# Performance work log

Hardware: AMD Instinct MI355X
Metric: run time of the kernel (lower is better)

Reference implementation:

```python
import jax, jax.numpy as jnp
import numpy as np


def _fwht_last(x):
    """Unnormalized Walsh-Hadamard transform along the last axis (len = power of 2)."""
    n = x.shape[-1]
    h = 1
    while h < n:
        x = x.reshape(*x.shape[:-1], n // (2 * h), 2, h)
        a, b = x[..., 0, :], x[..., 1, :]
        x = jnp.stack([a + b, a - b], axis=-2).reshape(*x.shape[:-3], n)
        h *= 2
    return x


def fwht(x, axis=-1):
    if axis in (-1, x.ndim - 1):
        return _fwht_last(x)
    return jnp.swapaxes(_fwht_last(jnp.swapaxes(x, axis, -1)), axis, -1)


def soft_threshold(x, T):
    return jnp.copysign(jax.nn.relu(jnp.abs(x) - jax.nn.relu(T)), x)


def setup_inputs() -> dict:
    key = jax.random.key(0)
    k1, k2, k3, k4 = jax.random.split(key, 4)
    B, C, H, W_dim = 32, 64, 128, 128
    x = jax.random.normal(k1, (B, C, H, W_dim), dtype=jnp.float32)
    W = jax.random.normal(k2, (C, C), dtype=jnp.float32) * 0.1  # 1x1 conv weight [out,in]
    v = jax.random.uniform(k3, (H, W_dim), dtype=jnp.float32)
    T = jax.random.uniform(k4, (H, W_dim), dtype=jnp.float32) * 0.1
    return {"x": x, "W": W, "v": v, "T": T}


def reference(x, W, v, T):
    H, Wd = x.shape[-2], x.shape[-1]
    # forward 2-D WHT (no padding: H, W already powers of 2)
    f2 = fwht(fwht(x, axis=-1), axis=-2)
    # spectral gate + 1x1 conv (channel mixing)
    f4 = jnp.einsum('oc,bchw->bohw', W, v * f2)
    # soft thresholding
    f6 = soft_threshold(f4, T)
    # inverse 2-D WHT = forward WHT / n along each axis
    y = fwht(fwht(f6, axis=-1), axis=-2) / (H * Wd)
    return y + x  # residual
```

## Files before the change

### kernel.cpp

```cpp
#include <hip/hip_runtime.h>
#include <math.h>

#define HW 16384
#define NPLANE 2048

typedef __bf16 bf16x8 __attribute__((ext_vector_type(8)));
typedef float  f32x4  __attribute__((ext_vector_type(4)));


__device__ __forceinline__ void bf_quad(float4& a) {
    float s0 = a.x + a.y, d0 = a.x - a.y;
    float s1 = a.z + a.w, d1 = a.z - a.w;
    a.x = s0 + s1; a.y = d0 + d1; a.z = s0 - s1; a.w = d0 - d1;
}

__device__ __forceinline__ void bf_pair(float4& a, float4& b) {
    float4 s, d;
    s.x = a.x + b.x; s.y = a.y + b.y; s.z = a.z + b.z; s.w = a.w + b.w;
    d.x = a.x - b.x; d.y = a.y - b.y; d.z = a.z - b.z; d.w = a.w - b.w;
    a = s; b = d;
}

__device__ __forceinline__ void bf_regs3(float4 (&r)[8]) {
    #pragma unroll
    for (int m = 1; m <= 4; m <<= 1) {
        #pragma unroll
        for (int j = 0; j < 8; ++j) {
            if (!(j & m)) bf_pair(r[j], r[j | m]);
        }
    }
}

__device__ __forceinline__ void wht14(const float* __restrict__ src,
                                      float* __restrict__ lds,
                                      float4 (&r)[8], int t) {
    const float4* s4 = reinterpret_cast<const float4*>(src);
    #pragma unroll
    for (int j = 0; j < 8; ++j) r[j] = s4[t + j * 512];
    #pragma unroll
    for (int j = 0; j < 8; ++j) bf_quad(r[j]);
    bf_regs3(r);

    {
        const int physT = (t & 3)
                        + ((((t >> 5) ^ (t >> 4)) & 1) << 4)
                        + (((t >> 6) & 7) << 5)
                        + (((t >> 2) & 7) << 8);
        const int swc = (t >> 2) & 3;
        #pragma unroll
        for (int j = 0; j < 8; ++j) {
            float* b = lds + physT + j * 2048;
            b[(0 ^ swc) << 2] = r[j].x;
            b[(1 ^ swc) << 2] = r[j].y;
            b[(2 ^ swc) << 2] = r[j].z;
            b[(3 ^ swc) << 2] = r[j].w;
        }
    }
    __syncthreads();

    {
        const int baseT = ((t & 63) << 2) + ((t >> 6) << 11);
        int addr[8];
        #pragma unroll
        for (int j = 0; j < 8; ++j) {
            addr[j] = (baseT ^ ((j & 3) << 2) ^ ((j >> 2) << 4)) + (j << 8);
            r[j] = *reinterpret_cast<const float4*>(lds + addr[j]);
        }
        #pragma unroll
        for (int j = 0; j < 8; ++j) bf_quad(r[j]);
        bf_regs3(r);
        #pragma unroll
        for (int j = 0; j < 8; ++j)
            *reinterpret_cast<float4*>(lds + addr[j]) = r[j];
    }
    __syncthreads();

    {
        const int t0 = t & 1, t1 = (t >> 1) & 1, t2 = (t >> 2) & 1;
        const int t3 = (t >> 3) & 1, t4 = (t >> 4) & 1, t5 = (t >> 5) & 1;
        const int cT = t1 + (t2 << 1) + ((t0 ^ t4) << 3)
                     + (t3 << 8) + (t4 << 9) + (t5 << 10) + ((t >> 6) << 11);
        #pragma unroll
        for (int j = 0; j < 8; ++j) {
            const int a = cT + ((((j >> 2) ^ t3)) << 2)
                        + ((j & 1) << 6) + (((j >> 1) & 1) << 7);
            float4 q;
            q.x = lds[a + ((0 ^ t5) << 4)];
            q.y = lds[a + ((1 ^ t5) << 4)];
            q.z = lds[a + ((0 ^ t5) << 4) + (1 << 5)];
            q.w = lds[a + ((1 ^ t5) << 4) + (1 << 5)];
            r[j] = q;
        }
        #pragma unroll
        for (int j = 0; j < 8; ++j) bf_quad(r[j]);
        #pragma unroll
        for (int m = 1; m <= 2; m <<= 1) {
            #pragma unroll
            for (int j = 0; j < 8; ++j) {
                if (!(j & m)) bf_pair(r[j], r[j | m]);
            }
        }
    }
}

__global__ __launch_bounds__(512) void k_wht2d_fwd(const float* __restrict__ x,
                                                   float* __restrict__ out) {
    __shared__ float lds[HW];
    const int t = threadIdx.x;
    const size_t plane = (size_t)blockIdx.x * HW;

    float4 r[8];
    wht14(x + plane, lds, r, t);

    float* dst = out + plane;
    const int dT = ((t & 63) << 1) + ((t >> 6) << 11);
    #pragma unroll
    for (int j = 0; j < 4; ++j) {
        const int jb = dT + ((j & 1) << 9) + ((j >> 1) << 10);
        const float* lo = reinterpret_cast<const float*>(&r[j]);
        const float* hi = reinterpret_cast<const float*>(&r[j + 4]);
        #pragma unroll
        for (int c = 0; c < 4; ++c) {
            const int d = jb + ((c & 1) << 7) + ((c >> 1) << 8);
            float2 o; o.x = lo[c]; o.y = hi[c];
            *reinterpret_cast<float2*>(dst + d) = o;
        }
    }
}

__global__ __launch_bounds__(512) void k_wht2d_inv(float* __restrict__ buf,
                                                   const float* __restrict__ x) {
    __shared__ float lds[HW];
    const int t = threadIdx.x;
    const size_t plane = (size_t)blockIdx.x * HW;

    float4 r[8];
    wht14(buf + plane, lds, r, t);

    float* dst = buf + plane;
    const float* xr = x + plane;
    const float s = 1.0f / 16384.0f;
    const int dT = ((t & 63) << 1) + ((t >> 6) << 11);
    #pragma unroll
    for (int j = 0; j < 4; ++j) {
        const int jb = dT + ((j & 1) << 9) + ((j >> 1) << 10);
        const float* lo = reinterpret_cast<const float*>(&r[j]);
        const float* hi = reinterpret_cast<const float*>(&r[j + 4]);
        #pragma unroll
        for (int c = 0; c < 4; ++c) {
            const int d = jb + ((c & 1) << 7) + ((c >> 1) << 8);
            float2 xv = *reinterpret_cast<const float2*>(xr + d);
            float2 o;
            o.x = lo[c] * s + xv.x;
            o.y = hi[c] * s + xv.y;
            *reinterpret_cast<float2*>(dst + d) = o;
        }
    }
}

__global__ __launch_bounds__(256) void k_mix_mfma(float* __restrict__ buf,
                                                  const float* __restrict__ W,
                                                  const float* __restrict__ v,
                                                  const float* __restrict__ T) {
    __shared__ float Xs[64 * 128];
    const int t = threadIdx.x;
    const int l = t & 63, w = t >> 6;
    const int b  = blockIdx.x >> 7;
    const int p0 = (blockIdx.x & 127) << 7;
    float* base = buf + (size_t)b * 64 * HW + p0;

    bf16x8 A[4][2];
    {
        const int row = l & 15;
        const int kc  = (l >> 4) * 8;
        #pragma unroll
        for (int mt = 0; mt < 4; ++mt) {
            const float* wr = W + (mt * 16 + row) * 64 + kc;
            #pragma unroll
            for (int ks = 0; ks < 2; ++ks) {
                float4 w0 = *reinterpret_cast<const float4*>(wr + ks * 32);
                float4 w1 = *reinterpret_cast<const float4*>(wr + ks * 32 + 4);
                bf16x8 a;
                a[0] = (__bf16)w0.x; a[1] = (__bf16)w0.y;
                a[2] = (__bf16)w0.z; a[3] = (__bf16)w0.w;
                a[4] = (__bf16)w1.x; a[5] = (__bf16)w1.y;
                a[6] = (__bf16)w1.z; a[7] = (__bf16)w1.w;
                A[mt][ks] = a;
            }
        }
    }

    #pragma unroll
    for (int i = 0; i < 8; ++i) {
        const int d  = i * 1024 + t * 4;
        const int c  = d >> 7;
        const int pq = d & 127;
        float4 xv = *reinterpret_cast<const float4*>(base + (size_t)c * HW + pq);
        float4 vv = *reinterpret_cast<const float4*>(v + p0 + pq);
        float4 r;
        r.x = xv.x * vv.x; r.y = xv.y * vv.y;
        r.z = xv.z * vv.z; r.w = xv.w * vv.w;
        const int gc = (c >> 3) & 3;
        *reinterpret_cast<float4*>(Xs + c * 128 + (pq ^ (gc << 4))) = r;
    }
    __syncthreads();

    f32x4 acc[4][2] = {};
    const int n0 = w * 32;
    const int g  = l >> 4;
    #pragma unroll
    for (int nt = 0; nt < 2; ++nt) {
        const int pl = n0 + nt * 16 + (l & 15);
        #pragma unroll
        for (int ks = 0; ks < 2; ++ks) {
            const float* col = Xs + (ks * 32 + g * 8) * 128 + (pl ^ (g << 4));
            bf16x8 bb;
            #pragma unroll
            for (int j = 0; j < 8; ++j) bb[j] = (__bf16)col[j * 128];
            #pragma unroll
            for (int mt = 0; mt < 4; ++mt)
                acc[mt][nt] = __builtin_amdgcn_mfma_f32_16x16x32_bf16(
                    A[mt][ks], bb, acc[mt][nt], 0, 0, 0);
        }
    }

    #pragma unroll
    for (int nt = 0; nt < 2; ++nt) {
        const int p  = p0 + n0 + nt * 16 + (l & 15);
        const float Tp = fmaxf(T[p], 0.0f);
        #pragma unroll
        for (int mt = 0; mt < 4; ++mt) {
            #pragma unroll
            for (int r = 0; r < 4; ++r) {
                const int o = mt * 16 + g * 4 + r;
                float val = acc[mt][nt][r];
                float mag = fmaxf(fabsf(val) - Tp, 0.0f);
                buf[(size_t)b * 64 * HW + (size_t)o * HW + p] = copysignf(mag, val);
            }
        }
    }
}

extern "C" void kernel_launch(void* const* d_in, const int* in_sizes, int n_in,
                              void* d_out, int out_size, void* d_ws, size_t ws_size,
                              hipStream_t stream) {
    const float* x = (const float*)d_in[0];
    const float* W = (const float*)d_in[1];
    const float* v = (const float*)d_in[2];
    const float* T = (const float*)d_in[3];
    float* out = (float*)d_out;

    k_wht2d_fwd<<<NPLANE, 512, 0, stream>>>(x, out);
    k_mix_mfma<<<32 * 128, 256, 0, stream>>>(out, W, v, T);
    k_wht2d_inv<<<NPLANE, 512, 0, stream>>>(out, x);
}
```

Baseline: 151.1 us.

## Process four planes per block with software-prefetch of next plane in WHT kernels

The forward and inverse WHT kernels now handle four 128x128 planes per workgroup, launching 512 blocks instead of 2048. Each iteration loads the next plane into registers while the LDS butterfly phases of the current plane run, and the inverse kernel issues its residual loads early. Barriers become explicit s_barrier calls with lgkmcnt waits and scheduling fences. The aim is to hide global-load latency. In exchange, register pressure goes up (a second 8xfloat4 buffer plus 16 float2 residuals), and with fewer blocks there may be less parallelism to fill the GPU.

```diff
diff --git a/kernel.cpp b/kernel.cpp
--- a/kernel.cpp
+++ b/kernel.cpp
@@ -7,6 +7,13 @@
 typedef __bf16 bf16x8 __attribute__((ext_vector_type(8)));
 typedef float  f32x4  __attribute__((ext_vector_type(4)));
 
+
+__device__ __forceinline__ void wg_barrier() {
+    __builtin_amdgcn_sched_barrier(0);
+    asm volatile("s_waitcnt lgkmcnt(0)");
+    __builtin_amdgcn_s_barrier();
+    __builtin_amdgcn_sched_barrier(0);
+}
 
 __device__ __forceinline__ void bf_quad(float4& a) {
     float s0 = a.x + a.y, d0 = a.x - a.y;
@@ -31,74 +38,67 @@
     }
 }
 
-__device__ __forceinline__ void wht14(const float* __restrict__ src,
-                                      float* __restrict__ lds,
-                                      float4 (&r)[8], int t) {
-    const float4* s4 = reinterpret_cast<const float4*>(src);
-    #pragma unroll
-    for (int j = 0; j < 8; ++j) r[j] = s4[t + j * 512];
+__device__ __forceinline__ void phaseA(float* __restrict__ lds,
+                                       float4 (&r)[8], int t) {
     #pragma unroll
     for (int j = 0; j < 8; ++j) bf_quad(r[j]);
     bf_regs3(r);
-
-    {
-        const int physT = (t & 3)
-                        + ((((t >> 5) ^ (t >> 4)) & 1) << 4)
-                        + (((t >> 6) & 7) << 5)
-                        + (((t >> 2) & 7) << 8);
-        const int swc = (t >> 2) & 3;
+    const int physT = (t & 3)
+                    + ((((t >> 5) ^ (t >> 4)) & 1) << 4)
+                    + (((t >> 6) & 7) << 5)
+                    + (((t >> 2) & 7) << 8);
+    const int swc = (t >> 2) & 3;
+    #pragma unroll
+    for (int j = 0; j < 8; ++j) {
+        float* b = lds + physT + j * 2048;
+        b[(0 ^ swc) << 2] = r[j].x;
+        b[(1 ^ swc) << 2] = r[j].y;
+        b[(2 ^ swc) << 2] = r[j].z;
+        b[(3 ^ swc) << 2] = r[j].w;
+    }
+}
+
+__device__ __forceinline__ void phaseB(float* __restrict__ lds,
+                                       float4 (&r)[8], int t) {
+    const int baseT = ((t & 63) << 2) + ((t >> 6) << 11);
+    int addr[8];
+    #pragma unroll
+    for (int j = 0; j < 8; ++j) {
+        addr[j] = (baseT ^ ((j & 3) << 2) ^ ((j >> 2) << 4)) + (j << 8);
+        r[j] = *reinterpret_cast<const float4*>(lds + addr[j]);
+    }
+    #pragma unroll
+    for (int j = 0; j < 8; ++j) bf_quad(r[j]);
+    bf_regs3(r);
+    #pragma unroll
+    for (int j = 0; j < 8; ++j)
+        *reinterpret_cast<float4*>(lds + addr[j]) = r[j];
+}
+
+__device__ __forceinline__ void phaseC(const float* __restrict__ lds,
+                                       float4 (&r)[8], int t) {
+    const int t0 = t & 1, t1 = (t >> 1) & 1, t2 = (t >> 2) & 1;
+    const int t3 = (t >> 3) & 1, t4 = (t >> 4) & 1, t5 = (t >> 5) & 1;
+    const int cT = t1 + (t2 << 1) + ((t0 ^ t4) << 3)
+                 + (t3 << 8) + (t4 << 9) + (t5 << 10) + ((t >> 6) << 11);
+    #pragma unroll
+    for (int j = 0; j < 8; ++j) {
+        const int a = cT + ((((j >> 2) ^ t3)) << 2)
+                    + ((j & 1) << 6) + (((j >> 1) & 1) << 7);
+        float4 q;
+        q.x = lds[a + ((0 ^ t5) << 4)];
+        q.y = lds[a + ((1 ^ t5) << 4)];
+        q.z = lds[a + ((0 ^ t5) << 4) + (1 << 5)];
+        q.w = lds[a + ((1 ^ t5) << 4) + (1 << 5)];
+        r[j] = q;
+    }
+    #pragma unroll
+    for (int j = 0; j < 8; ++j) bf_quad(r[j]);
+    #pragma unroll
+    for (int m = 1; m <= 2; m <<= 1) {
         #pragma unroll
         for (int j = 0; j < 8; ++j) {
-            float* b = lds + physT + j * 2048;
-            b[(0 ^ swc) << 2] = r[j].x;
-            b[(1 ^ swc) << 2] = r[j].y;
-            b[(2 ^ swc) << 2] = r[j].z;
-            b[(3 ^ swc) << 2] = r[j].w;
-        }
-    }
-    __syncthreads();
-
-    {
-        const int baseT = ((t & 63) << 2) + ((t >> 6) << 11);
-        int addr[8];
-        #pragma unroll
-        for (int j = 0; j < 8; ++j) {
-            addr[j] = (baseT ^ ((j & 3) << 2) ^ ((j >> 2) << 4)) + (j << 8);
-            r[j] = *reinterpret_cast<const float4*>(lds + addr[j]);
-        }
-        #pragma unroll
-        for (int j = 0; j < 8; ++j) bf_quad(r[j]);
-        bf_regs3(r);
-        #pragma unroll
-        for (int j = 0; j < 8; ++j)
-            *reinterpret_cast<float4*>(lds + addr[j]) = r[j];
-    }
-    __syncthreads();
-
-    {
-        const int t0 = t & 1, t1 = (t >> 1) & 1, t2 = (t >> 2) & 1;
-        const int t3 = (t >> 3) & 1, t4 = (t >> 4) & 1, t5 = (t >> 5) & 1;
-        const int cT = t1 + (t2 << 1) + ((t0 ^ t4) << 3)
-                     + (t3 << 8) + (t4 << 9) + (t5 << 10) + ((t >> 6) << 11);
-        #pragma unroll
-        for (int j = 0; j < 8; ++j) {
-            const int a = cT + ((((j >> 2) ^ t3)) << 2)
-                        + ((j & 1) << 6) + (((j >> 1) & 1) << 7);
-            float4 q;
-            q.x = lds[a + ((0 ^ t5) << 4)];
-            q.y = lds[a + ((1 ^ t5) << 4)];
-            q.z = lds[a + ((0 ^ t5) << 4) + (1 << 5)];
-            q.w = lds[a + ((1 ^ t5) << 4) + (1 << 5)];
-            r[j] = q;
-        }
-        #pragma unroll
-        for (int j = 0; j < 8; ++j) bf_quad(r[j]);
-        #pragma unroll
-        for (int m = 1; m <= 2; m <<= 1) {
-            #pragma unroll
-            for (int j = 0; j < 8; ++j) {
-                if (!(j & m)) bf_pair(r[j], r[j | m]);
-            }
+            if (!(j & m)) bf_pair(r[j], r[j | m]);
         }
     }
 }
@@ -107,23 +107,47 @@
                                                    float* __restrict__ out) {
     __shared__ float lds[HW];
     const int t = threadIdx.x;
-    const size_t plane = (size_t)blockIdx.x * HW;
-
-    float4 r[8];
-    wht14(x + plane, lds, r, t);
-
-    float* dst = out + plane;
-    const int dT = ((t & 63) << 1) + ((t >> 6) << 11);
-    #pragma unroll
-    for (int j = 0; j < 4; ++j) {
-        const int jb = dT + ((j & 1) << 9) + ((j >> 1) << 10);
-        const float* lo = reinterpret_cast<const float*>(&r[j]);
-        const float* hi = reinterpret_cast<const float*>(&r[j + 4]);
-        #pragma unroll
-        for (int c = 0; c < 4; ++c) {
-            const int d = jb + ((c & 1) << 7) + ((c >> 1) << 8);
-            float2 o; o.x = lo[c]; o.y = hi[c];
-            *reinterpret_cast<float2*>(dst + d) = o;
+    const size_t base = (size_t)blockIdx.x * 4 * HW;
+
+    float4 r[8], nxt[8];
+    {
+        const float4* s4 = reinterpret_cast<const float4*>(x + base);
+        #pragma unroll
+        for (int j = 0; j < 8; ++j) r[j] = s4[t + j * 512];
+    }
+
+    #pragma unroll
+    for (int p = 0; p < 4; ++p) {
+        phaseA(lds, r, t);
+        if (p < 3) {
+            const float4* n4 =
+                reinterpret_cast<const float4*>(x + base + (size_t)(p + 1) * HW);
+            #pragma unroll
+            for (int j = 0; j < 8; ++j) nxt[j] = n4[t + j * 512];
+        }
+        wg_barrier();
+        phaseB(lds, r, t);
+        wg_barrier();
+        phaseC(lds, r, t);
+
+        float* dst = out + base + (size_t)p * HW;
+        const int dT = ((t & 63) << 1) + ((t >> 6) << 11);
+        #pragma unroll
+        for (int j = 0; j < 4; ++j) {
+            const int jb = dT + ((j & 1) << 9) + ((j >> 1) << 10);
+            const float* lo = reinterpret_cast<const float*>(&r[j]);
+            const float* hi = reinterpret_cast<const float*>(&r[j + 4]);
+            #pragma unroll
+            for (int c = 0; c < 4; ++c) {
+                const int d = jb + ((c & 1) << 7) + ((c >> 1) << 8);
+                float2 o; o.x = lo[c]; o.y = hi[c];
+                *reinterpret_cast<float2*>(dst + d) = o;
+            }
+        }
+        if (p < 3) {
+            wg_barrier();
+            #pragma unroll
+            for (int j = 0; j < 8; ++j) r[j] = nxt[j];
         }
     }
 }
@@ -132,28 +156,64 @@
                                                    const float* __restrict__ x) {
     __shared__ float lds[HW];
     const int t = threadIdx.x;
-    const size_t plane = (size_t)blockIdx.x * HW;
-
-    float4 r[8];
-    wht14(buf + plane, lds, r, t);
-
-    float* dst = buf + plane;
-    const float* xr = x + plane;
+    const size_t base = (size_t)blockIdx.x * 4 * HW;
     const float s = 1.0f / 16384.0f;
     const int dT = ((t & 63) << 1) + ((t >> 6) << 11);
-    #pragma unroll
-    for (int j = 0; j < 4; ++j) {
-        const int jb = dT + ((j & 1) << 9) + ((j >> 1) << 10);
-        const float* lo = reinterpret_cast<const float*>(&r[j]);
-        const float* hi = reinterpret_cast<const float*>(&r[j + 4]);
-        #pragma unroll
-        for (int c = 0; c < 4; ++c) {
-            const int d = jb + ((c & 1) << 7) + ((c >> 1) << 8);
-            float2 xv = *reinterpret_cast<const float2*>(xr + d);
-            float2 o;
-            o.x = lo[c] * s + xv.x;
-            o.y = hi[c] * s + xv.y;
-            *reinterpret_cast<float2*>(dst + d) = o;
+
+    float4 r[8], nxt[8];
+    {
+        const float4* s4 = reinterpret_cast<const float4*>(buf + base);
+        #pragma unroll
+        for (int j = 0; j < 8; ++j) r[j] = s4[t + j * 512];
+    }
+
+    #pragma unroll
+    for (int p = 0; p < 4; ++p) {
+        phaseA(lds, r, t);
+
+        float2 xres[16];
+        {
+            const float* xr = x + base + (size_t)p * HW;
+            #pragma unroll
+            for (int j = 0; j < 4; ++j) {
+                const int jb = dT + ((j & 1) << 9) + ((j >> 1) << 10);
+                #pragma unroll
+                for (int c = 0; c < 4; ++c)
+                    xres[j * 4 + c] = *reinterpret_cast<const float2*>(
+                        xr + jb + ((c & 1) << 7) + ((c >> 1) << 8));
+            }
+        }
+        if (p < 3) {
+            const float4* n4 =
+                reinterpret_cast<const float4*>(buf + base + (size_t)(p + 1) * HW);
+            #pragma unroll
+            for (int j = 0; j < 8; ++j) nxt[j] = n4[t + j * 512];
+        }
+        wg_barrier();
+        phaseB(lds, r, t);
+        wg_barrier();
+        phaseC(lds, r, t);
+
+        float* dst = buf + base + (size_t)p * HW;
+        #pragma unroll
+        for (int j = 0; j < 4; ++j) {
+            const int jb = dT + ((j & 1) << 9) + ((j >> 1) << 10);
+            const float* lo = reinterpret_cast<const float*>(&r[j]);
+            const float* hi = reinterpret_cast<const float*>(&r[j + 4]);
+            #pragma unroll
+            for (int c = 0; c < 4; ++c) {
+                const int d = jb + ((c & 1) << 7) + ((c >> 1) << 8);
+                float2 xv = xres[j * 4 + c];
+                float2 o;
+                o.x = lo[c] * s + xv.x;
+                o.y = hi[c] * s + xv.y;
+                *reinterpret_cast<float2*>(dst + d) = o;
+            }
+        }
+        if (p < 3) {
+            wg_barrier();
+            #pragma unroll
+            for (int j = 0; j < 8; ++j) r[j] = nxt[j];
         }
     }
 }
@@ -250,7 +310,7 @@
     const float* T = (const float*)d_in[3];
     float* out = (float*)d_out;
 
-    k_wht2d_fwd<<<NPLANE, 512, 0, stream>>>(x, out);
+    k_wht2d_fwd<<<512, 512, 0, stream>>>(x, out);
     k_mix_mfma<<<32 * 128, 256, 0, stream>>>(out, W, v, T);
-    k_wht2d_inv<<<NPLANE, 512, 0, stream>>>(out, x);
-}
+    k_wht2d_inv<<<512, 512, 0, stream>>>(out, x);
+}
```

After: 158.1 us. 4.6% more time.
